# Kernel tuning notes

Hardware: AMD Instinct MI355X
Metric: run time of the kernel (lower is better)

Reference implementation:

```python
import jax, jax.numpy as jnp
import numpy as np

D_MODEL, D_STATE, D_CONV, D_INNER = 768, 16, 4, 1536
B, L = 4, 4096


def setup_inputs() -> dict:
    key = jax.random.key(0)
    ks = jax.random.split(key, 9)
    s = 0.02
    return {
        "x": jax.random.normal(ks[0], (B, L, D_MODEL), jnp.float32),
        "w_in": jax.random.normal(ks[1], (2 * D_INNER, D_MODEL), jnp.float32) * s,
        "w_conv": jax.random.normal(ks[2], (D_INNER, 1, D_CONV), jnp.float32) * 0.2,
        "w_xproj": jax.random.normal(ks[3], (2 * D_STATE + 1, D_INNER), jnp.float32) * s,
        "w_dt": jax.random.normal(ks[4], (D_INNER, 1), jnp.float32) * s,
        "b_dt": jax.random.normal(ks[5], (D_INNER,), jnp.float32) * 0.1,
        "a_log": jnp.log(jnp.tile(jnp.arange(1, D_STATE + 1, dtype=jnp.float32), (D_INNER, 1))),
        "d_param": jnp.ones((D_INNER,), jnp.float32),
        "w_out": jax.random.normal(ks[6], (D_MODEL, D_INNER), jnp.float32) * s,
    }


def _mamba_fwd(x, w_in, w_conv, w_xproj, w_dt, b_dt, a_log, d_param, w_out):
    Lseq = x.shape[1]
    xz = x @ w_in.T                                  # [B,L,2*Di]
    xs, z = jnp.split(xz, 2, axis=-1)                # [B,L,Di] each
    # depthwise causal conv1d (padding=d_conv-1, then crop to L == left-pad causal)
    xc = xs.transpose(0, 2, 1)                       # [B,Di,L]
    xc = jax.lax.conv_general_dilated(
        xc, w_conv, window_strides=(1,), padding=[(D_CONV - 1, 0)],
        feature_group_count=D_INNER, dimension_numbers=("NCH", "OIH", "NCH"))
    xs = jax.nn.silu(xc.transpose(0, 2, 1))          # [B,L,Di]
    # selective SSM parameters
    proj = xs @ w_xproj.T                            # [B,L,1+2N]
    delta_raw = proj[..., :1]                        # [B,L,1]
    b_proj = proj[..., 1:1 + D_STATE]                # [B,L,N]
    c_proj = proj[..., 1 + D_STATE:]                 # [B,L,N]
    delta = jax.nn.softplus(delta_raw @ w_dt.T + b_dt)   # [B,L,Di]
    a_mat = -jnp.exp(a_log)                          # [Di,N]

    def step(h, inp):
        dt, bt, ct, xt = inp                         # [B,Di],[B,N],[B,N],[B,Di]
        a_bar = jnp.exp(dt[:, :, None] * a_mat)      # [B,Di,N]
        h = a_bar * h + dt[:, :, None] * bt[:, None, :] * xt[:, :, None]
        y = jnp.einsum("bn,bdn->bd", ct, h) + d_param * xt
        return h, y

    h0 = jnp.zeros((x.shape[0], D_INNER, D_STATE), x.dtype)
    # time-major inputs for scan
    inputs = (delta.transpose(1, 0, 2), b_proj.transpose(1, 0, 2),
              c_proj.transpose(1, 0, 2), xs.transpose(1, 0, 2))
    _, ys = jax.lax.scan(step, h0, inputs, length=Lseq)
    y = ys.transpose(1, 0, 2)                        # [B,L,Di]
    return (y * jax.nn.silu(z)) @ w_out.T            # [B,L,d_model]


def reference(x, w_in, w_conv, w_xproj, w_dt, b_dt, a_log, d_param, w_out):
    return _mamba_fwd(x, w_in, w_conv, w_xproj, w_dt, b_dt, a_log, d_param, w_out)
```

## Files before the change

### kernel.cpp

```cpp
#include <hip/hip_runtime.h>
#include <hip/hip_bf16.h>

#define D_MODEL 768
#define D_STATE 16
#define D_INNER 1536
#define BB 4
#define LL 4096

typedef __bf16 bf16_t;
typedef __bf16 bf16x8 __attribute__((ext_vector_type(8)));
typedef __bf16 bf16x4 __attribute__((ext_vector_type(4)));
typedef float f32x4 __attribute__((ext_vector_type(4)));

#define AS1 __attribute__((address_space(1)))
#define AS3 __attribute__((address_space(3)))

__global__ __launch_bounds__(256) void cvt_all(
    const float4* __restrict__ x4, bf16x4* __restrict__ xb4,
    const float* __restrict__ w_in, const float* __restrict__ w_out,
    const float* __restrict__ w_xproj, bf16_t* __restrict__ wibf,
    bf16_t* __restrict__ wobf, bf16_t* __restrict__ wxpbf) {
  int i = blockIdx.x * 256 + threadIdx.x;
  float4 v = x4[i];
  bf16x4 o;
  o[0] = (bf16_t)v.x; o[1] = (bf16_t)v.y; o[2] = (bf16_t)v.z; o[3] = (bf16_t)v.w;
  xb4[i] = o;
  if (i < 1179648) {
    wibf[i] = (bf16_t)w_in[i];
    wibf[i + 1179648] = (bf16_t)w_in[i + 1179648];
    wobf[i] = (bf16_t)w_out[i];
    if (i < 98304) {
      int row = i / 1536;
      wxpbf[i] = (row < 33) ? (bf16_t)w_xproj[i] : (bf16_t)0.f;
    }
  }
}

template <typename CT, bool GATE>
__global__ __launch_bounds__(256, 4) void gemm_bk64(
    const bf16_t* __restrict__ A, const bf16_t* __restrict__ B,
    CT* __restrict__ C, int K, int ldc, int ncols) {
  __shared__ __align__(16) bf16_t As[128 * 64];
  __shared__ __align__(16) bf16_t Bs[128 * 64];
  const int t = threadIdx.x;
  const int lane = t & 63;
  const int wid = t >> 6;
  const int wm = (wid >> 1) * 64;
  const int wn = (wid & 1) * 64;
  const long Mbase = (long)blockIdx.x * 128;
  const long Nbase = (long)blockIdx.y * 128;

  const int sr = t >> 3;
  const int sc = ((t & 7) ^ (sr & 7)) * 8;

  const bf16_t* ap[4];
  const bf16_t* bp[4];
#pragma unroll
  for (int h = 0; h < 4; ++h) {
    ap[h] = A + (Mbase + h * 32 + sr) * K + sc;
    bp[h] = B + (Nbase + h * 32 + sr) * K + sc;
  }

  f32x4 acc[4][4];
#pragma unroll
  for (int i = 0; i < 4; ++i)
#pragma unroll
    for (int j = 0; j < 4; ++j) acc[i][j] = (f32x4){0.f, 0.f, 0.f, 0.f};

  const int lrow = lane & 15;
  const int cs0 = ((lane >> 4) ^ (lrow & 7)) * 8;
  const int cs1 = ((4 + (lane >> 4)) ^ (lrow & 7)) * 8;

  for (int k0 = 0; k0 < K; k0 += 64) {
    if (k0) __syncthreads();
#pragma unroll
    for (int h = 0; h < 4; ++h) {
      __builtin_amdgcn_global_load_lds(
          (const AS1 unsigned int*)ap[h],
          (AS3 unsigned int*)(&As[(h * 256 + t) * 8]), 16, 0, 0);
      ap[h] += 64;
    }
#pragma unroll
    for (int h = 0; h < 4; ++h) {
      __builtin_amdgcn_global_load_lds(
          (const AS1 unsigned int*)bp[h],
          (AS3 unsigned int*)(&Bs[(h * 256 + t) * 8]), 16, 0, 0);
      bp[h] += 64;
    }
    __syncthreads();

#pragma unroll
    for (int s = 0; s < 2; ++s) {
      const int co = s ? cs1 : cs0;
      bf16x8 af[4], bfr[4];
#pragma unroll
      for (int i = 0; i < 4; ++i)
        af[i] = *(const bf16x8*)(&As[(wm + i * 16 + lrow) * 64 + co]);
#pragma unroll
      for (int j = 0; j < 4; ++j)
        bfr[j] = *(const bf16x8*)(&Bs[(wn + j * 16 + lrow) * 64 + co]);
#pragma unroll
      for (int i = 0; i < 4; ++i)
#pragma unroll
        for (int j = 0; j < 4; ++j)
          acc[i][j] = __builtin_amdgcn_mfma_f32_16x16x32_bf16(af[i], bfr[j], acc[i][j], 0, 0, 0);
    }
  }

  const int orow = (lane >> 4) * 4;
  const int ocol = lane & 15;
#pragma unroll
  for (int i = 0; i < 4; ++i) {
#pragma unroll
    for (int j = 0; j < 4; ++j) {
      int col = (int)Nbase + wn + j * 16 + ocol;
      if (col < ncols) {
        long rowb = Mbase + wm + i * 16 + orow;
#pragma unroll
        for (int r = 0; r < 4; ++r) {
          float v = acc[i][j][r];
          if (GATE && col >= 1536) v = v / (1.f + __expf(-v));
          C[(rowb + r) * (long)ldc + col] = (CT)v;
        }
      }
    }
  }
}

__global__ __launch_bounds__(256, 4) void gemm_xproj(
    const bf16_t* __restrict__ A, const bf16_t* __restrict__ B,
    float* __restrict__ Cp, int K, int Klen) {
  __shared__ __align__(16) bf16_t As[128 * 32];
  __shared__ __align__(16) bf16_t Bs[64 * 32];
  const int t = threadIdx.x;
  const int lane = t & 63;
  const int wid = t >> 6;
  const int wm = wid * 32;
  const long Mbase = (long)blockIdx.x * 128;
  const long koff = (long)blockIdx.z * Klen;
  float* C = Cp + (long)blockIdx.z * 540672;

  const int sr = t >> 2;
  const int sc = ((t & 3) ^ ((t >> 3) & 3)) * 8;

  const bf16_t* ap0 = A + (Mbase + sr) * K + koff + sc;
  const bf16_t* ap1 = ap0 + 64 * (long)K;
  const bf16_t* bp = B + (long)sr * K + koff + sc;

  f32x4 acc[2][4];
#pragma unroll
  for (int i = 0; i < 2; ++i)
#pragma unroll
    for (int j = 0; j < 4; ++j) acc[i][j] = (f32x4){0.f, 0.f, 0.f, 0.f};

  const int lrow = lane & 15;
  const int lchunk = (((lane >> 4)) ^ ((lrow >> 1) & 3)) * 8;

  for (int k0 = 0; k0 < Klen; k0 += 32) {
    if (k0) __syncthreads();
    __builtin_amdgcn_global_load_lds(
        (const AS1 unsigned int*)ap0,
        (AS3 unsigned int*)(&As[t * 8]), 16, 0, 0);
    __builtin_amdgcn_global_load_lds(
        (const AS1 unsigned int*)ap1,
        (AS3 unsigned int*)(&As[(256 + t) * 8]), 16, 0, 0);
    __builtin_amdgcn_global_load_lds(
        (const AS1 unsigned int*)bp,
        (AS3 unsigned int*)(&Bs[t * 8]), 16, 0, 0);
    ap0 += 32; ap1 += 32; bp += 32;
    __syncthreads();

    bf16x8 bfr[4];
#pragma unroll
    for (int j = 0; j < 4; ++j)
      bfr[j] = *(const bf16x8*)(&Bs[(j * 16 + lrow) * 32 + lchunk]);
#pragma unroll
    for (int i = 0; i < 2; ++i) {
      bf16x8 af = *(const bf16x8*)(&As[(wm + i * 16 + lrow) * 32 + lchunk]);
#pragma unroll
      for (int j = 0; j < 4; ++j)
        acc[i][j] = __builtin_amdgcn_mfma_f32_16x16x32_bf16(af, bfr[j], acc[i][j], 0, 0, 0);
    }
  }

  const int orow = (lane >> 4) * 4;
  const int ocol = lane & 15;
#pragma unroll
  for (int i = 0; i < 2; ++i) {
    long rowb = Mbase + wm + i * 16 + orow;
#pragma unroll
    for (int j = 0; j < 3; ++j) {
      int col = j * 16 + ocol;
      if (col < 33) {
#pragma unroll
        for (int r = 0; r < 4; ++r)
          C[(rowb + r) * 33L + col] = acc[i][j][r];
      }
    }
  }
}

__global__ __launch_bounds__(256) void conv_silu(const bf16_t* __restrict__ xz,
                                                 const float4* __restrict__ wconv,
                                                 bf16_t* __restrict__ xc) {
  long T = (long)blockIdx.x * 256 + threadIdx.x;
  int d = (int)(T % 1536);
  long r = T / 1536;
  int l0 = (int)(r & 511) * 8;
  long b = r >> 9;
  float4 w = wconv[d];
  const bf16_t* xs = xz + ((long)b * LL + l0) * 3072 + d;
  float v[11];
  if (l0 == 0) {
    v[0] = 0.f; v[1] = 0.f; v[2] = 0.f;
  } else {
    v[0] = (float)xs[-3 * 3072]; v[1] = (float)xs[-2 * 3072]; v[2] = (float)xs[-3072];
  }
#pragma unroll
  for (int j = 3; j < 11; ++j) v[j] = (float)xs[(j - 3) * 3072];
  bf16_t* o = xc + ((long)b * LL + l0) * 1536 + d;
#pragma unroll
  for (int i = 0; i < 8; ++i) {
    float acc = w.x * v[i];
    acc = fmaf(w.y, v[i + 1], acc);
    acc = fmaf(w.z, v[i + 2], acc);
    acc = fmaf(w.w, v[i + 3], acc);
    o[(long)i * 1536] = (bf16_t)(acc / (1.f + __expf(-acc)));
  }
}

__device__ __forceinline__ float softplus_f(float x) {
  return (x > 15.f) ? x : __logf(1.f + __expf(x));
}


__global__ __launch_bounds__(256) void scan_p1(
    const bf16_t* __restrict__ xc, const float* __restrict__ projp,
    const float* __restrict__ w_dt, const float* __restrict__ b_dt,
    float4* __restrict__ hend, float* __restrict__ Ssum) {
  __shared__ __align__(16) float prs_bc[64 * 32];
  __shared__ float prs_d[64];
  const int c = blockIdx.x;
  const int b = blockIdx.z;
  const int t = threadIdx.x;
  const int d = blockIdx.y * 256 + t;
  const long blbase = (long)b * LL + (long)c * 64;

  const float* s0 = projp + blbase * 33;
  const float* s1 = s0 + 540672;
  for (int i = t; i < 2112; i += 256) {
    int row = i / 33, col = i - row * 33;
    float v = s0[i] + s1[i];
    if (col == 0) prs_d[row] = v; else prs_bc[row * 32 + col - 1] = v;
  }
  __syncthreads();

  const float wdt = w_dt[d];
  const float bdt = b_dt[d];
  float h[16];
#pragma unroll
  for (int n = 0; n < 16; ++n) h[n] = 0.f;
  float S = 0.f;

  for (int l = 0; l < 64; ++l) {
    float delta = softplus_f(fmaf(prs_d[l], wdt, bdt));
    S += delta;
    float E = __expf(-delta);
    float xt = (float)xc[(blbase + l) * 1536 + d];
    float dx = delta * xt;
    const f32x4* bc = (const f32x4*)&prs_bc[l * 32];
    float ab = E;
#pragma unroll
    for (int q = 0; q < 4; ++q) {
      f32x4 Bq = bc[q];
#pragma unroll
      for (int k = 0; k < 4; ++k) {
        h[q * 4 + k] = fmaf(ab, h[q * 4 + k], dx * Bq[k]);
        ab *= E;
      }
    }
  }
  long ob = ((long)b * 64 + c) * 1536 + d;
#pragma unroll
  for (int q = 0; q < 4; ++q)
    hend[ob * 4 + q] = (float4){h[q * 4], h[q * 4 + 1], h[q * 4 + 2], h[q * 4 + 3]};
  Ssum[ob] = S;
}

__global__ __launch_bounds__(256) void scan_p2(float* __restrict__ hend,
                                               const float* __restrict__ Ssum,
                                               const float* __restrict__ a_log) {
  int idx = blockIdx.x * 256 + threadIdx.x;
  int n = idx & 15;
  int dn = idx >> 4;
  int d = dn % 1536;
  int b = dn / 1536;
  float a = -__expf(a_log[d * 16 + n]);
  float hs = 0.f;
  for (int c = 0; c < 64; ++c) {
    long ob = ((long)b * 64 + c) * 1536 + d;
    float e = hend[ob * 16 + n];
    float S = Ssum[ob];
    hend[ob * 16 + n] = hs;
    hs = fmaf(__expf(a * S), hs, e);
  }
}

__global__ __launch_bounds__(256) void scan_p3(
    const bf16_t* __restrict__ xc, const float* __restrict__ projp,
    const bf16_t* __restrict__ xz, const float* __restrict__ w_dt,
    const float* __restrict__ b_dt, const float* __restrict__ d_param,
    const float4* __restrict__ hstart, bf16_t* __restrict__ ymul) {
  __shared__ __align__(16) float prs_bc[64 * 32];
  __shared__ float prs_d[64];
  const int c = blockIdx.x;
  const int b = blockIdx.z;
  const int t = threadIdx.x;
  const int d = blockIdx.y * 256 + t;
  const long blbase = (long)b * LL + (long)c * 64;

  const float* s0 = projp + blbase * 33;
  const float* s1 = s0 + 540672;
  for (int i = t; i < 2112; i += 256) {
    int row = i / 33, col = i - row * 33;
    float v = s0[i] + s1[i];
    if (col == 0) prs_d[row] = v; else prs_bc[row * 32 + col - 1] = v;
  }
  __syncthreads();

  const float wdt = w_dt[d];
  const float bdt = b_dt[d];
  const float Dv = d_param[d];
  long ob = ((long)b * 64 + c) * 1536 + d;
  float h[16];
#pragma unroll
  for (int q = 0; q < 4; ++q) {
    float4 h4 = hstart[ob * 4 + q];
    h[q * 4] = h4.x; h[q * 4 + 1] = h4.y; h[q * 4 + 2] = h4.z; h[q * 4 + 3] = h4.w;
  }

  for (int l = 0; l < 64; ++l) {
    float delta = softplus_f(fmaf(prs_d[l], wdt, bdt));
    float E = __expf(-delta);
    float xt = (float)xc[(blbase + l) * 1536 + d];
    float dx = delta * xt;
    const f32x4* bc = (const f32x4*)&prs_bc[l * 32];
    float ab = E;
    float y = 0.f;
#pragma unroll
    for (int q = 0; q < 4; ++q) {
      f32x4 Bq = bc[q];
      f32x4 Cq = bc[q + 4];
#pragma unroll
      for (int k = 0; k < 4; ++k) {
        h[q * 4 + k] = fmaf(ab, h[q * 4 + k], dx * Bq[k]);
        y = fmaf(Cq[k], h[q * 4 + k], y);
        ab *= E;
      }
    }
    y = fmaf(Dv, xt, y);
    float gz = (float)xz[(blbase + l) * 3072 + 1536 + d];
    ymul[(blbase + l) * 1536 + d] = (bf16_t)(y * gz);
  }
}

extern "C" void kernel_launch(void* const* d_in, const int* in_sizes, int n_in,
                              void* d_out, int out_size, void* d_ws, size_t ws_size,
                              hipStream_t stream) {
  const float* x       = (const float*)d_in[0];
  const float* w_in    = (const float*)d_in[1];
  const float* w_conv  = (const float*)d_in[2];
  const float* w_xproj = (const float*)d_in[3];
  const float* w_dt    = (const float*)d_in[4];
  const float* b_dt    = (const float*)d_in[5];
  const float* a_log   = (const float*)d_in[6];
  const float* d_param = (const float*)d_in[7];
  const float* w_out   = (const float*)d_in[8];
  float* out = (float*)d_out;

  char* ws = (char*)d_ws;
  bf16_t* xz    = (bf16_t*)ws;  ws += 100663296;
  bf16_t* xc    = (bf16_t*)ws;  ws += 50331648;
  float*  projp = (float*)ws;   ws += 4325376;
  float*  hend  = (float*)ws;   ws += 25165824;
  float*  Ssum  = (float*)ws;   ws += 1572864;
  bf16_t* wobf  = (bf16_t*)ws;  ws += 2359296;
  bf16_t* wxpbf = (bf16_t*)ws;  ws += 196608;
  bf16_t* ymul  = (bf16_t*)ws;  ws += 50331648;
  bf16_t* xbf   = ymul;
  bf16_t* wibf  = ymul + 12582912;

  cvt_all<<<12288, 256, 0, stream>>>((const float4*)x, (bf16x4*)xbf,
                                     w_in, w_out, w_xproj, wibf, wobf, wxpbf);

  gemm_bk64<bf16_t, true><<<dim3(128, 24), 256, 0, stream>>>(
      xbf, wibf, xz, 768, 3072, 3072);

  conv_silu<<<12288, 256, 0, stream>>>(xz, (const float4*)w_conv, xc);

  gemm_xproj<<<dim3(128, 1, 2), 256, 0, stream>>>(xc, wxpbf, projp, 1536, 768);

  scan_p1<<<dim3(64, 6, 4), 256, 0, stream>>>(xc, projp, w_dt, b_dt,
                                              (float4*)hend, Ssum);
  scan_p2<<<384, 256, 0, stream>>>(hend, Ssum, a_log);
  scan_p3<<<dim3(64, 6, 4), 256, 0, stream>>>(xc, projp, xz, w_dt, b_dt, d_param,
                                              (const float4*)hend, ymul);

  gemm_bk64<float, false><<<dim3(128, 6), 256, 0, stream>>>(
      ymul, wobf, out, 1536, 768, 768);
}
```

Baseline: 424.5 us.

## Fuse depthwise conv+SiLU into x-projection GEMM and recompute conv in scans

Removes the standalone conv_silu kernel and the materialized xc buffer. The conv+SiLU is computed on the fly into LDS inside a new conv_xproj GEMM (no split-K, 64-row tiles), and the scan passes recompute the conv from xz instead of reading xc. The scans now read proj directly from global memory rather than staging it in shared memory. This saves the xc write/read and one launch, in exchange for recomputing the conv three times, making strided 3072-wide xz reads, and a GEMM grid of only 256 blocks.

After: 452.1 us. 6.5% more time.

```diff
diff --git a/kernel.cpp b/kernel.cpp
--- a/kernel.cpp
+++ b/kernel.cpp
@@ -127,105 +127,86 @@
   }
 }
 
-__global__ __launch_bounds__(256, 4) void gemm_xproj(
-    const bf16_t* __restrict__ A, const bf16_t* __restrict__ B,
-    float* __restrict__ Cp, int K, int Klen) {
-  __shared__ __align__(16) bf16_t As[128 * 32];
-  __shared__ __align__(16) bf16_t Bs[64 * 32];
+__global__ __launch_bounds__(256) void conv_xproj(
+    const bf16_t* __restrict__ xz, const float4* __restrict__ wconv,
+    const bf16_t* __restrict__ wxp, float* __restrict__ proj) {
+  __shared__ __align__(16) bf16_t As[64 * 64];
+  __shared__ __align__(16) bf16_t Bs[64 * 64];
   const int t = threadIdx.x;
   const int lane = t & 63;
   const int wid = t >> 6;
-  const int wm = wid * 32;
-  const long Mbase = (long)blockIdx.x * 128;
-  const long koff = (long)blockIdx.z * Klen;
-  float* C = Cp + (long)blockIdx.z * 540672;
-
-  const int sr = t >> 2;
-  const int sc = ((t & 3) ^ ((t >> 3) & 3)) * 8;
-
-  const bf16_t* ap0 = A + (Mbase + sr) * K + koff + sc;
-  const bf16_t* ap1 = ap0 + 64 * (long)K;
-  const bf16_t* bp = B + (long)sr * K + koff + sc;
-
-  f32x4 acc[2][4];
-#pragma unroll
-  for (int i = 0; i < 2; ++i)
-#pragma unroll
-    for (int j = 0; j < 4; ++j) acc[i][j] = (f32x4){0.f, 0.f, 0.f, 0.f};
+  const long Rbase = (long)blockIdx.x * 64;
+  const int l0 = (int)(Rbase & (LL - 1));
+
+  const int ch = t & 63;
+  const int rg = t >> 6;
+
+  const int brow = t >> 3;
+  const int bg = (t & 7) ^ (brow & 7);
+  const bf16_t* bsrc0 = wxp + (long)brow * 1536 + bg * 8;
+  const bf16_t* bsrc1 = wxp + (long)(32 + brow) * 1536 + bg * 8;
+
+  f32x4 acc[3];
+#pragma unroll
+  for (int j = 0; j < 3; ++j) acc[j] = (f32x4){0.f, 0.f, 0.f, 0.f};
 
   const int lrow = lane & 15;
-  const int lchunk = (((lane >> 4)) ^ ((lrow >> 1) & 3)) * 8;
-
-  for (int k0 = 0; k0 < Klen; k0 += 32) {
-    if (k0) __syncthreads();
+  const int quad = lane >> 4;
+  const int wm = wid * 16;
+
+  for (int kc = 0; kc < 24; ++kc) {
+    if (kc) __syncthreads();
     __builtin_amdgcn_global_load_lds(
-        (const AS1 unsigned int*)ap0,
-        (AS3 unsigned int*)(&As[t * 8]), 16, 0, 0);
+        (const AS1 unsigned int*)(bsrc0 + kc * 64),
+        (AS3 unsigned int*)(&Bs[t * 8]), 16, 0, 0);
     __builtin_amdgcn_global_load_lds(
-        (const AS1 unsigned int*)ap1,
-        (AS3 unsigned int*)(&As[(256 + t) * 8]), 16, 0, 0);
-    __builtin_amdgcn_global_load_lds(
-        (const AS1 unsigned int*)bp,
-        (AS3 unsigned int*)(&Bs[t * 8]), 16, 0, 0);
-    ap0 += 32; ap1 += 32; bp += 32;
+        (const AS1 unsigned int*)(bsrc1 + kc * 64),
+        (AS3 unsigned int*)(&Bs[(256 + t) * 8]), 16, 0, 0);
+
+    const int d = kc * 64 + ch;
+    const float4 w = wconv[d];
+    const bf16_t* xp = xz + (Rbase + rg * 16) * 3072 + d;
+    float v0, v1, v2;
+    if (l0 == 0 && rg == 0) {
+      v0 = 0.f; v1 = 0.f; v2 = 0.f;
+    } else {
+      v0 = (float)xp[-3 * 3072]; v1 = (float)xp[-2 * 3072]; v2 = (float)xp[-3072];
+    }
+#pragma unroll
+    for (int i = 0; i < 16; ++i) {
+      float cur = (float)xp[i * 3072];
+      float a = w.x * v0;
+      a = fmaf(w.y, v1, a);
+      a = fmaf(w.z, v2, a);
+      a = fmaf(w.w, cur, a);
+      float s = a / (1.f + __expf(-a));
+      int r = rg * 16 + i;
+      As[r * 64 + (((ch >> 3) ^ (r & 7))) * 8 + (ch & 7)] = (bf16_t)s;
+      v0 = v1; v1 = v2; v2 = cur;
+    }
     __syncthreads();
 
-    bf16x8 bfr[4];
-#pragma unroll
-    for (int j = 0; j < 4; ++j)
-      bfr[j] = *(const bf16x8*)(&Bs[(j * 16 + lrow) * 32 + lchunk]);
-#pragma unroll
-    for (int i = 0; i < 2; ++i) {
-      bf16x8 af = *(const bf16x8*)(&As[(wm + i * 16 + lrow) * 32 + lchunk]);
-#pragma unroll
-      for (int j = 0; j < 4; ++j)
-        acc[i][j] = __builtin_amdgcn_mfma_f32_16x16x32_bf16(af, bfr[j], acc[i][j], 0, 0, 0);
-    }
-  }
-
-  const int orow = (lane >> 4) * 4;
-  const int ocol = lane & 15;
-#pragma unroll
-  for (int i = 0; i < 2; ++i) {
-    long rowb = Mbase + wm + i * 16 + orow;
-#pragma unroll
-    for (int j = 0; j < 3; ++j) {
-      int col = j * 16 + ocol;
-      if (col < 33) {
-#pragma unroll
-        for (int r = 0; r < 4; ++r)
-          C[(rowb + r) * 33L + col] = acc[i][j][r];
+#pragma unroll
+    for (int s = 0; s < 2; ++s) {
+      const int co = ((s * 4 + quad) ^ (lrow & 7)) * 8;
+      bf16x8 af = *(const bf16x8*)(&As[(wm + lrow) * 64 + co]);
+#pragma unroll
+      for (int j = 0; j < 3; ++j) {
+        bf16x8 bfr = *(const bf16x8*)(&Bs[(j * 16 + lrow) * 64 + co]);
+        acc[j] = __builtin_amdgcn_mfma_f32_16x16x32_bf16(af, bfr, acc[j], 0, 0, 0);
       }
     }
   }
-}
-
-__global__ __launch_bounds__(256) void conv_silu(const bf16_t* __restrict__ xz,
-                                                 const float4* __restrict__ wconv,
-                                                 bf16_t* __restrict__ xc) {
-  long T = (long)blockIdx.x * 256 + threadIdx.x;
-  int d = (int)(T % 1536);
-  long r = T / 1536;
-  int l0 = (int)(r & 511) * 8;
-  long b = r >> 9;
-  float4 w = wconv[d];
-  const bf16_t* xs = xz + ((long)b * LL + l0) * 3072 + d;
-  float v[11];
-  if (l0 == 0) {
-    v[0] = 0.f; v[1] = 0.f; v[2] = 0.f;
-  } else {
-    v[0] = (float)xs[-3 * 3072]; v[1] = (float)xs[-2 * 3072]; v[2] = (float)xs[-3072];
-  }
-#pragma unroll
-  for (int j = 3; j < 11; ++j) v[j] = (float)xs[(j - 3) * 3072];
-  bf16_t* o = xc + ((long)b * LL + l0) * 1536 + d;
-#pragma unroll
-  for (int i = 0; i < 8; ++i) {
-    float acc = w.x * v[i];
-    acc = fmaf(w.y, v[i + 1], acc);
-    acc = fmaf(w.z, v[i + 2], acc);
-    acc = fmaf(w.w, v[i + 3], acc);
-    o[(long)i * 1536] = (bf16_t)(acc / (1.f + __expf(-acc)));
+
+#pragma unroll
+  for (int j = 0; j < 3; ++j) {
+    int col = j * 16 + lrow;
+    if (col < 33) {
+      long rowb = Rbase + wm + quad * 4;
+#pragma unroll
+      for (int r = 0; r < 4; ++r)
+        proj[(rowb + r) * 33L + col] = acc[j][r];
+    }
   }
 }
 
@@ -235,47 +216,52 @@
 
 
 __global__ __launch_bounds__(256) void scan_p1(
-    const bf16_t* __restrict__ xc, const float* __restrict__ projp,
-    const float* __restrict__ w_dt, const float* __restrict__ b_dt,
-    float4* __restrict__ hend, float* __restrict__ Ssum) {
-  __shared__ __align__(16) float prs_bc[64 * 32];
-  __shared__ float prs_d[64];
+    const bf16_t* __restrict__ xz, const float4* __restrict__ wconv,
+    const float* __restrict__ proj, const float* __restrict__ w_dt,
+    const float* __restrict__ b_dt, float4* __restrict__ hend,
+    float* __restrict__ Ssum) {
   const int c = blockIdx.x;
   const int b = blockIdx.z;
   const int t = threadIdx.x;
   const int d = blockIdx.y * 256 + t;
   const long blbase = (long)b * LL + (long)c * 64;
 
-  const float* s0 = projp + blbase * 33;
-  const float* s1 = s0 + 540672;
-  for (int i = t; i < 2112; i += 256) {
-    int row = i / 33, col = i - row * 33;
-    float v = s0[i] + s1[i];
-    if (col == 0) prs_d[row] = v; else prs_bc[row * 32 + col - 1] = v;
-  }
-  __syncthreads();
-
+  const float4 w = wconv[d];
   const float wdt = w_dt[d];
   const float bdt = b_dt[d];
+  const bf16_t* xp = xz + blbase * 3072 + d;
+  float v0, v1, v2;
+  if (c == 0) {
+    v0 = 0.f; v1 = 0.f; v2 = 0.f;
+  } else {
+    v0 = (float)xp[-3 * 3072]; v1 = (float)xp[-2 * 3072]; v2 = (float)xp[-3072];
+  }
+
   float h[16];
 #pragma unroll
   for (int n = 0; n < 16; ++n) h[n] = 0.f;
   float S = 0.f;
 
   for (int l = 0; l < 64; ++l) {
-    float delta = softplus_f(fmaf(prs_d[l], wdt, bdt));
+    float cur = (float)xp[(long)l * 3072];
+    float a = w.x * v0;
+    a = fmaf(w.y, v1, a);
+    a = fmaf(w.z, v2, a);
+    a = fmaf(w.w, cur, a);
+    float xt = a / (1.f + __expf(-a));
+    v0 = v1; v1 = v2; v2 = cur;
+
+    const float* pr = proj + (blbase + l) * 33;
+    float delta = softplus_f(fmaf(pr[0], wdt, bdt));
     S += delta;
     float E = __expf(-delta);
-    float xt = (float)xc[(blbase + l) * 1536 + d];
     float dx = delta * xt;
-    const f32x4* bc = (const f32x4*)&prs_bc[l * 32];
     float ab = E;
 #pragma unroll
     for (int q = 0; q < 4; ++q) {
-      f32x4 Bq = bc[q];
 #pragma unroll
       for (int k = 0; k < 4; ++k) {
-        h[q * 4 + k] = fmaf(ab, h[q * 4 + k], dx * Bq[k]);
+        h[q * 4 + k] = fmaf(ab, h[q * 4 + k], dx * pr[1 + q * 4 + k]);
         ab *= E;
       }
     }
@@ -307,30 +293,28 @@
 }
 
 __global__ __launch_bounds__(256) void scan_p3(
-    const bf16_t* __restrict__ xc, const float* __restrict__ projp,
-    const bf16_t* __restrict__ xz, const float* __restrict__ w_dt,
+    const bf16_t* __restrict__ xz, const float4* __restrict__ wconv,
+    const float* __restrict__ proj, const float* __restrict__ w_dt,
     const float* __restrict__ b_dt, const float* __restrict__ d_param,
     const float4* __restrict__ hstart, bf16_t* __restrict__ ymul) {
-  __shared__ __align__(16) float prs_bc[64 * 32];
-  __shared__ float prs_d[64];
   const int c = blockIdx.x;
   const int b = blockIdx.z;
   const int t = threadIdx.x;
   const int d = blockIdx.y * 256 + t;
   const long blbase = (long)b * LL + (long)c * 64;
 
-  const float* s0 = projp + blbase * 33;
-  const float* s1 = s0 + 540672;
-  for (int i = t; i < 2112; i += 256) {
-    int row = i / 33, col = i - row * 33;
-    float v = s0[i] + s1[i];
-    if (col == 0) prs_d[row] = v; else prs_bc[row * 32 + col - 1] = v;
-  }
-  __syncthreads();
-
+  const float4 w = wconv[d];
   const float wdt = w_dt[d];
   const float bdt = b_dt[d];
   const float Dv = d_param[d];
+  const bf16_t* xp = xz + blbase * 3072 + d;
+  float v0, v1, v2;
+  if (c == 0) {
+    v0 = 0.f; v1 = 0.f; v2 = 0.f;
+  } else {
+    v0 = (float)xp[-3 * 3072]; v1 = (float)xp[-2 * 3072]; v2 = (float)xp[-3072];
+  }
+
   long ob = ((long)b * 64 + c) * 1536 + d;
   float h[16];
 #pragma unroll
@@ -340,26 +324,31 @@
   }
 
   for (int l = 0; l < 64; ++l) {
-    float delta = softplus_f(fmaf(prs_d[l], wdt, bdt));
+    float cur = (float)xp[(long)l * 3072];
+    float a = w.x * v0;
+    a = fmaf(w.y, v1, a);
+    a = fmaf(w.z, v2, a);
+    a = fmaf(w.w, cur, a);
+    float xt = a / (1.f + __expf(-a));
+    v0 = v1; v1 = v2; v2 = cur;
+
+    const float* pr = proj + (blbase + l) * 33;
+    float delta = softplus_f(fmaf(pr[0], wdt, bdt));
     float E = __expf(-delta);
-    float xt = (float)xc[(blbase + l) * 1536 + d];
     float dx = delta * xt;
-    const f32x4* bc = (const f32x4*)&prs_bc[l * 32];
     float ab = E;
     float y = 0.f;
 #pragma unroll
     for (int q = 0; q < 4; ++q) {
-      f32x4 Bq = bc[q];
-      f32x4 Cq = bc[q + 4];
 #pragma unroll
       for (int k = 0; k < 4; ++k) {
-        h[q * 4 + k] = fmaf(ab, h[q * 4 + k], dx * Bq[k]);
-        y = fmaf(Cq[k], h[q * 4 + k], y);
+        h[q * 4 + k] = fmaf(ab, h[q * 4 + k], dx * pr[1 + q * 4 + k]);
+        y = fmaf(pr[17 + q * 4 + k], h[q * 4 + k], y);
         ab *= E;
       }
     }
     y = fmaf(Dv, xt, y);
-    float gz = (float)xz[(blbase + l) * 3072 + 1536 + d];
+    float gz = (float)xp[(long)l * 3072 + 1536];
     ymul[(blbase + l) * 1536 + d] = (bf16_t)(y * gz);
   }
 }
@@ -380,8 +369,7 @@
 
   char* ws = (char*)d_ws;
   bf16_t* xz    = (bf16_t*)ws;  ws += 100663296;
-  bf16_t* xc    = (bf16_t*)ws;  ws += 50331648;
-  float*  projp = (float*)ws;   ws += 4325376;
+  float*  proj  = (float*)ws;   ws += 2162688;
   float*  hend  = (float*)ws;   ws += 25165824;
   float*  Ssum  = (float*)ws;   ws += 1572864;
   bf16_t* wobf  = (bf16_t*)ws;  ws += 2359296;
@@ -396,14 +384,13 @@
   gemm_bk64<bf16_t, true><<<dim3(128, 24), 256, 0, stream>>>(
       xbf, wibf, xz, 768, 3072, 3072);
 
-  conv_silu<<<12288, 256, 0, stream>>>(xz, (const float4*)w_conv, xc);
-
-  gemm_xproj<<<dim3(128, 1, 2), 256, 0, stream>>>(xc, wxpbf, projp, 1536, 768);
-
-  scan_p1<<<dim3(64, 6, 4), 256, 0, stream>>>(xc, projp, w_dt, b_dt,
-                                              (float4*)hend, Ssum);
+  conv_xproj<<<256, 256, 0, stream>>>(xz, (const float4*)w_conv, wxpbf, proj);
+
+  scan_p1<<<dim3(64, 6, 4), 256, 0, stream>>>(xz, (const float4*)w_conv, proj,
+                                              w_dt, b_dt, (float4*)hend, Ssum);
   scan_p2<<<384, 256, 0, stream>>>(hend, Ssum, a_log);
-  scan_p3<<<dim3(64, 6, 4), 256, 0, stream>>>(xc, projp, xz, w_dt, b_dt, d_param,
+  scan_p3<<<dim3(64, 6, 4), 256, 0, stream>>>(xz, (const float4*)w_conv, proj,
+                                              w_dt, b_dt, d_param,
                                               (const float4*)hend, ymul);
 
   gemm_bk64<float, false><<<dim3(128, 6), 256, 0, stream>>>(
```
